# Performance work log

Hardware: AMD Instinct MI355X
Metric: run time of the kernel (lower is better)

Reference implementation:

```python
import jax, jax.numpy as jnp
import numpy as np

N = 100000   # nodes
E = 625000   # edges
H = 128      # hidden dim
G = 64       # graphs in batch
HOPS = 5
EPS = 1e-5


def _gelu(x):
    return jax.nn.gelu(x, approximate=False)  # torch nn.GELU default (exact erf)


def _bn(x, g, b):
    # BatchNorm1d in training mode: batch statistics, biased variance
    m = jnp.mean(x, axis=0)
    v = jnp.var(x, axis=0)
    return (x - m) * jax.lax.rsqrt(v + EPS) * g + b


def _ffnn(x, W1, b1, W2, b2):
    # Linear -> GELU -> Linear -> GELU
    return _gelu(_gelu(x @ W1 + b1) @ W2 + b2)


def _vn_mlp(x, W1, b1, g1, be1, W2, b2, g2, be2):
    # Linear -> BN -> GELU -> Linear -> BN -> GELU
    h = _gelu(_bn(x @ W1 + b1, g1, be1))
    return _gelu(_bn(h @ W2 + b2, g2, be2))


def _gcn(x, W, b, src, dst):
    # PyG GCNConv: xW, symmetric-normalized aggregation over edges w/ self loops, + bias
    h = x @ W
    deg = jax.ops.segment_sum(jnp.ones_like(src, dtype=h.dtype), dst, num_segments=N)
    dinv = jax.lax.rsqrt(jnp.maximum(deg, 1.0))  # deg >= 1 due to self loops
    norm = dinv[src] * dinv[dst]                 # [E+N]
    out = jax.ops.segment_sum(h[src] * norm[:, None], dst, num_segments=N)
    return out + b


def _forward(x, edge_index, batch, pre_W1, pre_b1, pre_W2, pre_b2, conv_W, conv_b,
             bn_g, bn_b, ffn_W1, ffn_b1, ffn_W2, ffn_b2, vn_W1, vn_b1, vn_g1, vn_be1,
             vn_W2, vn_b2, vn_g2, vn_be2, vn_emb, post_W1, post_b1, post_W2, post_b2):
    loop = jnp.arange(N)
    src = jnp.concatenate([edge_index[0], loop])
    dst = jnp.concatenate([edge_index[1], loop])

    x = _ffnn(x.astype(jnp.float32), pre_W1, pre_b1, pre_W2, pre_b2)
    vn = jnp.broadcast_to(vn_emb[0], (G, H))  # vn(zeros(num_graphs))

    counts = jax.ops.segment_sum(jnp.ones((N,), x.dtype), batch, num_segments=G)
    inv_counts = 1.0 / jnp.maximum(counts, 1.0)

    for i in range(HOPS):
        x = x + vn[batch]
        x = _gcn(x, conv_W[i], conv_b[i], src, dst) + x
        x = _bn(x, bn_g[i], bn_b[i])
        x = _ffnn(x, ffn_W1[i], ffn_b1[i], ffn_W2[i], ffn_b2[i]) + x
        # dropout p=0.0 -> identity
        if i < HOPS - 1:
            pooled = jax.ops.segment_sum(x, batch, num_segments=G) * inv_counts[:, None]
            vn = vn + pooled
            vn = _vn_mlp(vn, vn_W1[i], vn_b1[i], vn_g1[i], vn_be1[i],
                         vn_W2[i], vn_b2[i], vn_g2[i], vn_be2[i])

    x = jax.ops.segment_sum(x, batch, num_segments=G)  # global_add_pool
    return _ffnn(x, post_W1, post_b1, post_W2, post_b2)


def setup_inputs():
    key = jax.random.key(0)
    ks = iter(jax.random.split(key, 40))
    def nrm(shape, s=0.05):
        return jax.random.normal(next(ks), shape, dtype=jnp.float32) * s
    d = {}
    d["x"] = jax.random.normal(next(ks), (N, H), dtype=jnp.float32)
    d["edge_index"] = jax.random.randint(next(ks), (2, E), 0, N)
    d["batch"] = jnp.sort(jax.random.randint(next(ks), (N,), 0, G))
    d["pre_W1"] = nrm((H, 2 * H)); d["pre_b1"] = jnp.zeros((2 * H,), jnp.float32)
    d["pre_W2"] = nrm((2 * H, H)); d["pre_b2"] = jnp.zeros((H,), jnp.float32)
    d["conv_W"] = nrm((HOPS, H, H)); d["conv_b"] = jnp.zeros((HOPS, H), jnp.float32)
    d["bn_g"] = jnp.ones((HOPS, H), jnp.float32); d["bn_b"] = jnp.zeros((HOPS, H), jnp.float32)
    d["ffn_W1"] = nrm((HOPS, H, 2 * H)); d["ffn_b1"] = jnp.zeros((HOPS, 2 * H), jnp.float32)
    d["ffn_W2"] = nrm((HOPS, 2 * H, H)); d["ffn_b2"] = jnp.zeros((HOPS, H), jnp.float32)
    d["vn_W1"] = nrm((HOPS - 1, H, 2 * H)); d["vn_b1"] = jnp.zeros((HOPS - 1, 2 * H), jnp.float32)
    d["vn_g1"] = jnp.ones((HOPS - 1, 2 * H), jnp.float32); d["vn_be1"] = jnp.zeros((HOPS - 1, 2 * H), jnp.float32)
    d["vn_W2"] = nrm((HOPS - 1, 2 * H, H)); d["vn_b2"] = jnp.zeros((HOPS - 1, H), jnp.float32)
    d["vn_g2"] = jnp.ones((HOPS - 1, H), jnp.float32); d["vn_be2"] = jnp.zeros((HOPS - 1, H), jnp.float32)
    d["vn_emb"] = nrm((1, H))
    d["post_W1"] = nrm((H, 2 * H)); d["post_b1"] = jnp.zeros((2 * H,), jnp.float32)
    d["post_W2"] = nrm((2 * H, H)); d["post_b2"] = jnp.zeros((H,), jnp.float32)
    return d


def reference(x, edge_index, batch, pre_W1, pre_b1, pre_W2, pre_b2, conv_W, conv_b,
              bn_g, bn_b, ffn_W1, ffn_b1, ffn_W2, ffn_b2, vn_W1, vn_b1, vn_g1, vn_be1,
              vn_W2, vn_b2, vn_g2, vn_be2, vn_emb, post_W1, post_b1, post_W2, post_b2):
    return _forward(x, edge_index, batch, pre_W1, pre_b1, pre_W2, pre_b2, conv_W, conv_b,
                    bn_g, bn_b, ffn_W1, ffn_b1, ffn_W2, ffn_b2, vn_W1, vn_b1, vn_g1, vn_be1,
                    vn_W2, vn_b2, vn_g2, vn_be2, vn_emb, post_W1, post_b1, post_W2, post_b2)
```

## Files before the change

### kernel.cpp

```cpp
#include <hip/hip_runtime.h>
#include <math.h>

#define H 128
#define H2 256
#define LDC 136

typedef __attribute__((ext_vector_type(8))) short short8;
typedef __attribute__((ext_vector_type(4))) float floatx4;

__device__ __forceinline__ float gelu_f(float x) {
  float t = 1.59576912161f * x * fmaf(0.044715f, x * x, 1.0f);
  return x / (1.0f + __expf(-t));
}

__device__ __forceinline__ unsigned short f2b(float f) {
  union { float f; unsigned u; } c; c.f = f;
  unsigned r = c.u + 0x7fffu + ((c.u >> 16) & 1u);
  return (unsigned short)(r >> 16);
}

__device__ __forceinline__ float b2f(unsigned short u) {
  union { unsigned u; float f; } c; c.u = ((unsigned)u) << 16; return c.f;
}

__device__ __forceinline__ short8 pack8(floatx4 a, floatx4 b) {
  union { short8 v; unsigned short s[8]; } u;
  u.s[0] = f2b(a.x); u.s[1] = f2b(a.y); u.s[2] = f2b(a.z); u.s[3] = f2b(a.w);
  u.s[4] = f2b(b.x); u.s[5] = f2b(b.y); u.s[6] = f2b(b.z); u.s[7] = f2b(b.w);
  return u.v;
}

__global__ __launch_bounds__(256) void transpose_w(const float* __restrict__ W, unsigned short* __restrict__ WT,
                                                   int K, int Ncol, int total) {
  int i = blockIdx.x * 256 + threadIdx.x;
  if (i >= total) return;
  int kn = K * Ncol;
  int b = i / kn, r = i - b * kn;
  int k = r / Ncol, n = r - k * Ncol;
  WT[b * kn + n * K + k] = f2b(W[i]);
}


__global__ __launch_bounds__(256) void hist_kernel(int* __restrict__ cnt, const int* __restrict__ dst, int E) {
  int i = blockIdx.x * 256 + threadIdx.x;
  if (i < E) atomicAdd(&cnt[dst[i]], 1);
}

__global__ __launch_bounds__(256) void scan_a(const int* __restrict__ cnt, int* __restrict__ row_ptr,
                                              int* __restrict__ blockSum, float* __restrict__ dinv, int N) {
  __shared__ int ls[256];
  int t = threadIdx.x;
  int idx = blockIdx.x * 1024 + t * 4;
  int4 v = make_int4(0, 0, 0, 0);
  if (idx + 3 < N) v = *(const int4*)&cnt[idx];
  else {
    if (idx + 0 < N) v.x = cnt[idx + 0];
    if (idx + 1 < N) v.y = cnt[idx + 1];
    if (idx + 2 < N) v.z = cnt[idx + 2];
    if (idx + 3 < N) v.w = cnt[idx + 3];
  }
  if (idx + 0 < N) dinv[idx + 0] = rsqrtf((float)v.x + 1.0f);
  if (idx + 1 < N) dinv[idx + 1] = rsqrtf((float)v.y + 1.0f);
  if (idx + 2 < N) dinv[idx + 2] = rsqrtf((float)v.z + 1.0f);
  if (idx + 3 < N) dinv[idx + 3] = rsqrtf((float)v.w + 1.0f);
  int s = v.x + v.y + v.z + v.w;
  ls[t] = s;
  __syncthreads();
  for (int off = 1; off < 256; off <<= 1) {
    int a = (t >= off) ? ls[t - off] : 0;
    __syncthreads();
    ls[t] += a;
    __syncthreads();
  }
  int p = ls[t] - s;
  if (t == 255) blockSum[blockIdx.x] = ls[255];
  if (idx + 0 < N) row_ptr[idx + 0] = p;  p += v.x;
  if (idx + 1 < N) row_ptr[idx + 1] = p;  p += v.y;
  if (idx + 2 < N) row_ptr[idx + 2] = p;  p += v.z;
  if (idx + 3 < N) row_ptr[idx + 3] = p;
}

__global__ __launch_bounds__(1024) void scan_b(const int* __restrict__ blockSum, int* __restrict__ blockOff,
                                               int nb, int* __restrict__ row_ptr, int N, int E) {
  __shared__ int ls[1024];
  int t = threadIdx.x;
  int s = (t < nb) ? blockSum[t] : 0;
  ls[t] = s;
  __syncthreads();
  for (int off = 1; off < 1024; off <<= 1) {
    int a = (t >= off) ? ls[t - off] : 0;
    __syncthreads();
    ls[t] += a;
    __syncthreads();
  }
  if (t < nb) blockOff[t] = ls[t] - s;
  if (t == 0) row_ptr[N] = E;
}

__global__ __launch_bounds__(256) void scan_c(int* __restrict__ row_ptr, const int* __restrict__ blockOff, int N) {
  int t = threadIdx.x;
  int idx = blockIdx.x * 1024 + t * 4;
  int off = blockOff[blockIdx.x];
  if (off == 0) return;
  if (idx + 3 < N) {
    int4 v = *(const int4*)&row_ptr[idx];
    v.x += off; v.y += off; v.z += off; v.w += off;
    *(int4*)&row_ptr[idx] = v;
  } else {
    if (idx + 0 < N) row_ptr[idx + 0] += off;
    if (idx + 1 < N) row_ptr[idx + 1] += off;
    if (idx + 2 < N) row_ptr[idx + 2] += off;
    if (idx + 3 < N) row_ptr[idx + 3] += off;
  }
}

__global__ __launch_bounds__(256) void build_csr_kernel(const int* __restrict__ src, const int* __restrict__ dst,
                                                        const int* __restrict__ row_ptr, int* __restrict__ cursor,
                                                        const float* __restrict__ dinv,
                                                        int* __restrict__ csr_src, float* __restrict__ csr_norm,
                                                        int E) {
  int i = blockIdx.x * 256 + threadIdx.x;
  if (i < E) {
    int s = src[i], d = dst[i];
    int pos = row_ptr[d] + atomicAdd(&cursor[d], 1);
    csr_src[pos] = s;
    csr_norm[pos] = dinv[s] * dinv[d];
  }
}


__global__ __launch_bounds__(256) void count_kernel(float* counts, const int* __restrict__ batch, int N, int G) {
  __shared__ float hist[256];
  int t = threadIdx.x;
  if (t < G) hist[t] = 0.f;
  __syncthreads();
  int i0 = (blockIdx.x * 256 + t) * 16;
  int cur = -1; float run = 0.f;
  for (int j = 0; j < 16; j++) {
    int i = i0 + j;
    if (i < N) {
      int b = batch[i];
      if (b == cur) run += 1.f;
      else { if (cur >= 0) atomicAdd(&hist[cur], run); cur = b; run = 1.f; }
    }
  }
  if (cur >= 0) atomicAdd(&hist[cur], run);
  __syncthreads();
  if (t < G && hist[t] != 0.f) atomicAdd(&counts[t], hist[t]);
}

__global__ __launch_bounds__(256) void vn_init_kernel(float* vn, const float* __restrict__ emb, int n) {
  int i = blockIdx.x * 256 + threadIdx.x;
  if (i < n) vn[i] = emb[i & (H - 1)];
}

__global__ __launch_bounds__(256) void gather_agg(const unsigned short* __restrict__ h, const int* __restrict__ csr_src,
                                                  const float* __restrict__ csr_norm, const int* __restrict__ row_ptr,
                                                  const float* __restrict__ dinv, const float* __restrict__ vn,
                                                  const int* __restrict__ batch, const float* __restrict__ bias,
                                                  float* __restrict__ x, float* __restrict__ stats, int N) {
  __shared__ float sred[4 * H];
  __shared__ float qred[4 * H];
  int w = threadIdx.x >> 6, lane = threadIdx.x & 63;
  int c = lane * 2;
  float2 bi = *(const float2*)&bias[c];
  float s0t = 0.f, s1t = 0.f, q0t = 0.f, q1t = 0.f;
  int base = blockIdx.x * 32 + w * 8;
  for (int j = 0; j < 8; j++) {
    int node = base + j;
    if (node >= N) break;
    int b = batch[node];
    float di = dinv[node];
    float2 xo = *(const float2*)&x[(long)node * H + c];
    float2 vv = *(const float2*)&vn[b * H + c];
    unsigned hv = *(const unsigned*)&h[(long)node * H + c];
    int beg = row_ptr[node], end = row_ptr[node + 1];
    float ax = b2f((unsigned short)hv) * di * di;
    float ay = b2f((unsigned short)(hv >> 16)) * di * di;
    for (int e = beg; e < end; e += 8) {
      int si[8]; float wg[8]; unsigned u[8];
#pragma unroll
      for (int i = 0; i < 8; i++) {
        int ee = e + i;
        bool in = ee < end;
        int idx = in ? ee : beg;
        si[i] = csr_src[idx];
        wg[i] = in ? csr_norm[idx] : 0.f;
      }
#pragma unroll
      for (int i = 0; i < 8; i++) u[i] = *(const unsigned*)&h[(long)si[i] * H + c];
#pragma unroll
      for (int i = 0; i < 8; i++) {
        ax += b2f((unsigned short)u[i]) * wg[i];
        ay += b2f((unsigned short)(u[i] >> 16)) * wg[i];
      }
    }
    float rx = ax + xo.x + vv.x + bi.x;
    float ry = ay + xo.y + vv.y + bi.y;
    *(float2*)&x[(long)node * H + c] = make_float2(rx, ry);
    s0t += rx; q0t += rx * rx;
    s1t += ry; q1t += ry * ry;
  }
  sred[w * H + c] = s0t; sred[w * H + c + 1] = s1t;
  qred[w * H + c] = q0t; qred[w * H + c + 1] = q1t;
  __syncthreads();
  int t = threadIdx.x;
  if (t < H) {
    float s = sred[t] + sred[H + t] + sred[2 * H + t] + sred[3 * H + t];
    if (s != 0.f) atomicAdd(&stats[t], s);
  } else {
    int cc = t - H;
    float q = qred[cc] + qred[H + cc] + qred[2 * H + cc] + qred[3 * H + cc];
    if (q != 0.f) atomicAdd(&stats[H + cc], q);
  }
}

__global__ __launch_bounds__(128) void bn_finalize_kernel(const float* __restrict__ stats, const float* __restrict__ g,
                                                          const float* __restrict__ b, float* __restrict__ scsh,
                                                          float invN) {
  int c = threadIdx.x;
  float m = stats[c] * invN;
  float v = stats[H + c] * invN - m * m;
  float sc = rsqrtf(v + 1e-5f) * g[c];
  scsh[c] = sc;
  scsh[H + c] = b[c] - m * sc;
}

__global__ __launch_bounds__(256) void conv_gemm(const float* __restrict__ x, const unsigned short* __restrict__ BT,
                                                 const float* __restrict__ vn, const int* __restrict__ batch,
                                                 unsigned short* __restrict__ h16, int M) {
  __shared__ unsigned short Bs[H * LDC];
  int tid = threadIdx.x;
  int lane = tid & 63, w = tid >> 6;
  int row0 = blockIdx.x * 64;
  int mrow = lane & 15, quad = lane >> 4, cn = lane & 15;
  int arow = row0 + w * 16 + mrow;
  bool rin = arow < M;
  int b = rin ? batch[arow] : 0;

#pragma unroll
  for (int j = 0; j < 8; j++) {
    int chunk = j * 256 + tid;
    int n = chunk >> 4, k8 = (chunk & 15) * 8;
    *(short8*)&Bs[n * LDC + k8] = *(const short8*)&BT[(long)n * H + k8];
  }

  short8 af[4];
#pragma unroll
  for (int k0 = 0; k0 < 4; k0++) {
    int kb = k0 * 32 + quad * 8;
    floatx4 a0 = (floatx4)0.f, a1 = (floatx4)0.f;
    if (rin) {
      a0 = *(const floatx4*)&x[(long)arow * H + kb] + *(const floatx4*)&vn[b * H + kb];
      a1 = *(const floatx4*)&x[(long)arow * H + kb + 4] + *(const floatx4*)&vn[b * H + kb + 4];
    }
    af[k0] = pack8(a0, a1);
  }
  __syncthreads();

#pragma unroll
  for (int t = 0; t < 8; t++) {
    floatx4 a = (floatx4)0.f;
#pragma unroll
    for (int k0 = 0; k0 < 4; k0++) {
      int kb = k0 * 32 + quad * 8;
      short8 bf = *(const short8*)&Bs[(t * 16 + mrow) * LDC + kb];
      a = __builtin_amdgcn_mfma_f32_16x16x32_bf16(af[k0], bf, a, 0, 0, 0);
    }
    int c = t * 16 + cn;
#pragma unroll
    for (int i = 0; i < 4; i++) {
      int r = row0 + w * 16 + quad * 4 + i;
      if (r < M) h16[(long)r * H + c] = f2b(a[i]);
    }
  }
}

template <int BNRES, int POOL>
__global__ __launch_bounds__(1024) void ffn_persist(const float* __restrict__ A,
                                                    const unsigned short* __restrict__ W1T, const float* __restrict__ b1,
                                                    const unsigned short* __restrict__ W2T, const float* __restrict__ b2,
                                                    const float* __restrict__ scsh,
                                                    float* __restrict__ C, float* __restrict__ pooled,
                                                    const int* __restrict__ batch, int M) {
  __shared__ unsigned short lds[78848];
  int tid = threadIdx.x;
#pragma unroll
  for (int j = 0; j < 4; j++) {
    int idx = j * 1024 + tid;
    int n = idx >> 4, k8 = (idx & 15) * 8;
    *(short8*)&lds[n * 136 + k8] = *(const short8*)&W1T[n * 128 + k8];
  }
#pragma unroll
  for (int j = 0; j < 4; j++) {
    int idx = j * 1024 + tid;
    int n = idx >> 5, k8 = (idx & 31) * 8;
    *(short8*)&lds[34816 + n * 264 + k8] = *(const short8*)&W2T[n * 256 + k8];
  }
  __syncthreads();

  int lane = tid & 63, w = tid >> 6;
  int mrow = lane & 15, quad = lane >> 4, cn = lane & 15;
  unsigned short* scr = &lds[68608 + w * 640];
  int TT = (M + 15) >> 4;
  int stride = (int)(gridDim.x << 4);

  for (int tile = blockIdx.x * 16 + w; tile < TT; tile += stride) {
    int row0 = tile << 4;
    int arow = row0 + mrow;
    bool rin = arow < M;

    short8 af[4];
#pragma unroll
    for (int k0 = 0; k0 < 4; k0++) {
      int kb = k0 * 32 + quad * 8;
      floatx4 a0 = (floatx4)0.f, a1 = (floatx4)0.f;
      if (rin) {
        a0 = *(const floatx4*)&A[(long)arow * H + kb];
        a1 = *(const floatx4*)&A[(long)arow * H + kb + 4];
        if (BNRES) {
          a0 = a0 * *(const floatx4*)&scsh[kb] + *(const floatx4*)&scsh[H + kb];
          a1 = a1 * *(const floatx4*)&scsh[kb + 4] + *(const floatx4*)&scsh[H + kb + 4];
        }
      }
      af[k0] = pack8(a0, a1);
    }

    floatx4 acc2[8];
#pragma unroll
    for (int t = 0; t < 8; t++) acc2[t] = (floatx4)0.f;

#pragma unroll
    for (int p = 0; p < 8; p++) {
#pragma unroll
      for (int u = 0; u < 2; u++) {
        int t = p * 2 + u;
        floatx4 a = (floatx4)0.f;
#pragma unroll
        for (int k = 0; k < 4; k++) {
          short8 bf = *(const short8*)&lds[(t * 16 + mrow) * 136 + k * 32 + quad * 8];
          a = __builtin_amdgcn_mfma_f32_16x16x32_bf16(af[k], bf, a, 0, 0, 0);
        }
        float bb = b1[t * 16 + cn];
#pragma unroll
        for (int i = 0; i < 4; i++)
          scr[(quad * 4 + i) * 40 + u * 16 + cn] = f2b(gelu_f(a[i] + bb));
      }
      short8 hf = *(const short8*)&scr[mrow * 40 + quad * 8];
#pragma unroll
      for (int ct = 0; ct < 8; ct++) {
        short8 bf = *(const short8*)&lds[34816 + (ct * 16 + mrow) * 264 + p * 32 + quad * 8];
        acc2[ct] = __builtin_amdgcn_mfma_f32_16x16x32_bf16(hf, bf, acc2[ct], 0, 0, 0);
      }
    }

    int g0 = 0; bool same = true;
    if (POOL) {
      int rl = row0 + 15; if (rl >= M) rl = M - 1;
      g0 = batch[row0];
      same = (batch[rl] == g0);
    }
#pragma unroll
    for (int t = 0; t < 8; t++) {
      int c = t * 16 + cn;
      float bb = b2[c];
      float rsc = 0.f, rsh = 0.f;
      if (BNRES) { rsc = scsh[c]; rsh = scsh[H + c]; }
      float s = 0.f;
#pragma unroll
      for (int i = 0; i < 4; i++) {
        int r = row0 + quad * 4 + i;
        float v = 0.f;
        if (r < M) {
          long off = (long)r * H + c;
          v = gelu_f(acc2[t][i] + bb);
          if (BNRES) v += C[off] * rsc + rsh;
          C[off] = v;
          if (POOL && !same) atomicAdd(&pooled[batch[r] * H + c], v);
        }
        s += v;
      }
      if (POOL && same) {
        s += __shfl_xor(s, 16);
        s += __shfl_xor(s, 32);
        if (quad == 0) atomicAdd(&pooled[g0 * H + c], s);
      }
    }
  }
}

template <int BN, int UVN>
__global__ __launch_bounds__(256) void mlp64_l1(const float* __restrict__ vn, const float* __restrict__ pooled,
                                                const float* __restrict__ counts,
                                                const float* __restrict__ W1, const float* __restrict__ b1,
                                                const float* __restrict__ g1, const float* __restrict__ be1,
                                                float* __restrict__ h1) {
  __shared__ float u[64 * H];
  __shared__ float red[8 * 64];
  int t = threadIdx.x;
  for (int idx = t; idx < 64 * H; idx += 256) {
    float v = pooled[idx];
    if (UVN) v = vn[idx] + v / fmaxf(counts[idx >> 7], 1.0f);
    u[idx] = v;
  }
  __syncthreads();
  int tc = t & 63, tg = t >> 6;
  int c = blockIdx.x * 64 + tc;
  float acc[16];
  float bj = b1[c];
#pragma unroll
  for (int g = 0; g < 16; g++) acc[g] = bj;
  for (int k0 = 0; k0 < H; k0 += 4) {
    float w0 = W1[(k0 + 0) * H2 + c];
    float w1 = W1[(k0 + 1) * H2 + c];
    float w2 = W1[(k0 + 2) * H2 + c];
    float w3 = W1[(k0 + 3) * H2 + c];
#pragma unroll
    for (int g = 0; g < 16; g++) {
      float4 v = *(const float4*)&u[(tg * 16 + g) * H + k0];
      acc[g] += v.x * w0 + v.y * w1 + v.z * w2 + v.w * w3;
    }
  }
  float sc = 1.f, sh = 0.f;
  if (BN) {
    float s = 0.f, s2 = 0.f;
#pragma unroll
    for (int g = 0; g < 16; g++) { s += acc[g]; s2 += acc[g] * acc[g]; }
    red[tg * 64 + tc] = s;
    red[256 + tg * 64 + tc] = s2;
    __syncthreads();
    float st = red[tc] + red[64 + tc] + red[128 + tc] + red[192 + tc];
    float st2 = red[256 + tc] + red[320 + tc] + red[384 + tc] + red[448 + tc];
    float m = st * (1.f / 64.f);
    float var = st2 * (1.f / 64.f) - m * m;
    sc = rsqrtf(var + 1e-5f) * g1[c];
    sh = be1[c] - m * sc;
  }
#pragma unroll
  for (int g = 0; g < 16; g++) h1[(tg * 16 + g) * H2 + c] = gelu_f(acc[g] * sc + sh);
}

template <int BN>
__global__ __launch_bounds__(256) void mlp64_l2(const float* __restrict__ h1,
                                                const float* __restrict__ W2, const float* __restrict__ b2,
                                                const float* __restrict__ g2, const float* __restrict__ be2,
                                                float* __restrict__ outp) {
  __shared__ float red[8 * 64];
  int t = threadIdx.x;
  int tc = t & 63, tg = t >> 6;
  int c = blockIdx.x * 64 + tc;
  float acc[16];
  float bj = b2[c];
#pragma unroll
  for (int g = 0; g < 16; g++) acc[g] = bj;
  for (int k0 = 0; k0 < H2; k0 += 4) {
    float w0 = W2[(k0 + 0) * H + c];
    float w1 = W2[(k0 + 1) * H + c];
    float w2 = W2[(k0 + 2) * H + c];
    float w3 = W2[(k0 + 3) * H + c];
#pragma unroll
    for (int g = 0; g < 16; g++) {
      float4 v = *(const float4*)&h1[(tg * 16 + g) * H2 + k0];
      acc[g] += v.x * w0 + v.y * w1 + v.z * w2 + v.w * w3;
    }
  }
  float sc = 1.f, sh = 0.f;
  if (BN) {
    float s = 0.f, s2 = 0.f;
#pragma unroll
    for (int g = 0; g < 16; g++) { s += acc[g]; s2 += acc[g] * acc[g]; }
    red[tg * 64 + tc] = s;
    red[256 + tg * 64 + tc] = s2;
    __syncthreads();
    float st = red[tc] + red[64 + tc] + red[128 + tc] + red[192 + tc];
    float st2 = red[256 + tc] + red[320 + tc] + red[384 + tc] + red[448 + tc];
    float m = st * (1.f / 64.f);
    float var = st2 * (1.f / 64.f) - m * m;
    sc = rsqrtf(var + 1e-5f) * g2[c];
    sh = be2[c] - m * sc;
  }
#pragma unroll
  for (int g = 0; g < 16; g++) outp[(tg * 16 + g) * H + c] = gelu_f(acc[g] * sc + sh);
}


extern "C" void kernel_launch(void* const* d_in, const int* in_sizes, int n_in,
                              void* d_out, int out_size, void* d_ws, size_t ws_size,
                              hipStream_t stream) {
  const float* x_in   = (const float*)d_in[0];
  const int*   edge   = (const int*)d_in[1];
  const int*   batch  = (const int*)d_in[2];
  const float* pre_W1 = (const float*)d_in[3];
  const float* pre_b1 = (const float*)d_in[4];
  const float* pre_W2 = (const float*)d_in[5];
  const float* pre_b2 = (const float*)d_in[6];
  const float* conv_W = (const float*)d_in[7];
  const float* conv_b = (const float*)d_in[8];
  const float* bn_g   = (const float*)d_in[9];
  const float* bn_b   = (const float*)d_in[10];
  const float* ffn_W1 = (const float*)d_in[11];
  const float* ffn_b1 = (const float*)d_in[12];
  const float* ffn_W2 = (const float*)d_in[13];
  const float* ffn_b2 = (const float*)d_in[14];
  const float* vn_W1  = (const float*)d_in[15];
  const float* vn_b1  = (const float*)d_in[16];
  const float* vn_g1  = (const float*)d_in[17];
  const float* vn_be1 = (const float*)d_in[18];
  const float* vn_W2  = (const float*)d_in[19];
  const float* vn_b2  = (const float*)d_in[20];
  const float* vn_g2  = (const float*)d_in[21];
  const float* vn_be2 = (const float*)d_in[22];
  const float* vn_emb = (const float*)d_in[23];
  const float* post_W1= (const float*)d_in[24];
  const float* post_b1= (const float*)d_in[25];
  const float* post_W2= (const float*)d_in[26];
  const float* post_b2= (const float*)d_in[27];
  float* out = (float*)d_out;

  const int N    = in_sizes[2];
  const int E    = in_sizes[1] / 2;
  const int G    = out_size / H;
  const int HOPS = in_sizes[7] / (H * H);
  const int NH   = N * H;

  float* w = (float*)d_ws;
  float* buf_x  = w;  w += NH;
  float* buf_t  = w;  w += N * H2;
  unsigned short* buf_h16 = (unsigned short*)buf_t;
  float* dinv   = w;  w += N;
  float* counts = w;  w += G;
  float* stats  = w;  w += 2 * H;
  float* scsh   = w;  w += 2 * H;
  float* pooled = w;  w += G * H;
  float* vn     = w;  w += G * H;
  float* mlp_h1 = w;  w += G * H2;
  float* csr_norm = w; w += E;
  int* iw = (int*)w;
  int* cnt      = iw;  iw += N;
  int* row_ptr  = iw;  iw += N + 1;
  int* cursor   = iw;  iw += N;
  int* csr_src  = iw;  iw += E;
  int* blockSum = iw;  iw += 1024;
  int* blockOff = iw;  iw += 1024;
  unsigned short* wt = (unsigned short*)iw;
  unsigned short* preW1T = wt;  wt += H * H2;
  unsigned short* preW2T = wt;  wt += H2 * H;
  unsigned short* convT  = wt;  wt += HOPS * H * H;
  unsigned short* ffn1T  = wt;  wt += HOPS * H * H2;
  unsigned short* ffn2T  = wt;  wt += HOPS * H2 * H;

  const int* src = edge;
  const int* dst = edge + E;

  int gE  = (E + 255) / 256;
  int gM  = (N + 63) / 64;
  int nb  = (N + 1023) / 1024;
  float invN = 1.0f / (float)N;

  transpose_w<<<(H * H2 + 255) / 256, 256, 0, stream>>>(pre_W1, preW1T, H, H2, H * H2);
  transpose_w<<<(H2 * H + 255) / 256, 256, 0, stream>>>(pre_W2, preW2T, H2, H, H2 * H);
  transpose_w<<<(HOPS * H * H + 255) / 256, 256, 0, stream>>>(conv_W, convT, H, H, HOPS * H * H);
  transpose_w<<<(HOPS * H * H2 + 255) / 256, 256, 0, stream>>>(ffn_W1, ffn1T, H, H2, HOPS * H * H2);
  transpose_w<<<(HOPS * H2 * H + 255) / 256, 256, 0, stream>>>(ffn_W2, ffn2T, H2, H, HOPS * H2 * H);

  hipMemsetAsync(cnt, 0, N * sizeof(int), stream);
  hist_kernel<<<gE, 256, 0, stream>>>(cnt, dst, E);
  scan_a<<<nb, 256, 0, stream>>>(cnt, row_ptr, blockSum, dinv, N);
  scan_b<<<1, 1024, 0, stream>>>(blockSum, blockOff, nb, row_ptr, N, E);
  scan_c<<<nb, 256, 0, stream>>>(row_ptr, blockOff, N);
  hipMemsetAsync(cursor, 0, N * sizeof(int), stream);
  build_csr_kernel<<<gE, 256, 0, stream>>>(src, dst, row_ptr, cursor, dinv, csr_src, csr_norm, E);

  hipMemsetAsync(counts, 0, G * sizeof(float), stream);
  count_kernel<<<(N + 256 * 16 - 1) / (256 * 16), 256, 0, stream>>>(counts, batch, N, G);
  vn_init_kernel<<<(G * H + 255) / 256, 256, 0, stream>>>(vn, vn_emb, G * H);

  ffn_persist<0, 0><<<256, 1024, 0, stream>>>(x_in, preW1T, pre_b1, preW2T, pre_b2, nullptr,
                                              buf_x, nullptr, nullptr, N);

  for (int i = 0; i < HOPS; i++) {
    conv_gemm<<<gM, 256, 0, stream>>>(buf_x, convT + i * H * H, vn, batch, buf_h16, N);
    hipMemsetAsync(stats, 0, 2 * H * sizeof(float), stream);
    gather_agg<<<(N + 31) / 32, 256, 0, stream>>>(buf_h16, csr_src, csr_norm, row_ptr, dinv, vn, batch,
                                                  conv_b + i * H, buf_x, stats, N);
    bn_finalize_kernel<<<1, 128, 0, stream>>>(stats, bn_g + i * H, bn_b + i * H, scsh, invN);
    hipMemsetAsync(pooled, 0, G * H * sizeof(float), stream);
    ffn_persist<1, 1><<<256, 1024, 0, stream>>>(buf_x, ffn1T + i * H * H2, ffn_b1 + i * H2,
                                                ffn2T + i * H2 * H, ffn_b2 + i * H, scsh,
                                                buf_x, pooled, batch, N);
    if (i < HOPS - 1) {
      mlp64_l1<1, 1><<<H2 / 64, 256, 0, stream>>>(vn, pooled, counts,
                                                  vn_W1 + i * H * H2, vn_b1 + i * H2, vn_g1 + i * H2, vn_be1 + i * H2,
                                                  mlp_h1);
      mlp64_l2<1><<<H / 64, 256, 0, stream>>>(mlp_h1, vn_W2 + i * H2 * H, vn_b2 + i * H, vn_g2 + i * H, vn_be2 + i * H, vn);
    }
  }

  mlp64_l1<0, 0><<<H2 / 64, 256, 0, stream>>>(nullptr, pooled, nullptr, post_W1, post_b1, nullptr, nullptr, mlp_h1);
  mlp64_l2<0><<<H / 64, 256, 0, stream>>>(mlp_h1, post_W2, post_b2, nullptr, nullptr, out);
}
```

Baseline: 1.778 ms.

## Restructure gather aggregation for multi-node ILP and prefetch FFN tiles

The gather kernel now has each wave handle two nodes at once with 4-wide channel vectors. It processes four node groups per half-wave in an interleaved way, loading CSR indices cooperatively and broadcasting them with shuffles, so more independent gathers are in flight. conv_gemm issues its x loads before the weight staging into LDS. ffn_persist prefetches the next tile's A rows into registers and batches the residual reads and output stores, which overlaps global latency with MFMA work. The cost is higher register pressure, which may lower occupancy, plus some wasted loads on inactive lanes.

```diff
diff --git a/kernel.cpp b/kernel.cpp
--- a/kernel.cpp
+++ b/kernel.cpp
@@ -22,6 +22,9 @@
 __device__ __forceinline__ float b2f(unsigned short u) {
   union { unsigned u; float f; } c; c.u = ((unsigned)u) << 16; return c.f;
 }
+
+__device__ __forceinline__ float blo(unsigned u) { return __uint_as_float(u << 16); }
+__device__ __forceinline__ float bhi(unsigned u) { return __uint_as_float(u & 0xffff0000u); }
 
 __device__ __forceinline__ short8 pack8(floatx4 a, floatx4 b) {
   union { short8 v; unsigned short s[8]; } u;
@@ -162,47 +165,130 @@
   __shared__ float sred[4 * H];
   __shared__ float qred[4 * H];
   int w = threadIdx.x >> 6, lane = threadIdx.x & 63;
-  int c = lane * 2;
-  float2 bi = *(const float2*)&bias[c];
-  float s0t = 0.f, s1t = 0.f, q0t = 0.f, q1t = 0.f;
+  int hh = lane >> 5;
+  int li = lane & 31;
+  int c = li * 4;
+  floatx4 bi = *(const floatx4*)&bias[c];
   int base = blockIdx.x * 32 + w * 8;
-  for (int j = 0; j < 8; j++) {
-    int node = base + j;
-    if (node >= N) break;
-    int b = batch[node];
-    float di = dinv[node];
-    float2 xo = *(const float2*)&x[(long)node * H + c];
-    float2 vv = *(const float2*)&vn[b * H + c];
-    unsigned hv = *(const unsigned*)&h[(long)node * H + c];
-    int beg = row_ptr[node], end = row_ptr[node + 1];
-    float ax = b2f((unsigned short)hv) * di * di;
-    float ay = b2f((unsigned short)(hv >> 16)) * di * di;
-    for (int e = beg; e < end; e += 8) {
-      int si[8]; float wg[8]; unsigned u[8];
-#pragma unroll
-      for (int i = 0; i < 8; i++) {
-        int ee = e + i;
-        bool in = ee < end;
-        int idx = in ? ee : beg;
-        si[i] = csr_src[idx];
-        wg[i] = in ? csr_norm[idx] : 0.f;
+
+  int nd[4]; bool act[4];
+#pragma unroll
+  for (int j = 0; j < 4; j++) {
+    int n0 = base + 2 * j + hh;
+    act[j] = n0 < N;
+    nd[j] = act[j] ? n0 : (N - 1);
+  }
+  int beg[4], end[4], bt[4];
+  float dd[4];
+#pragma unroll
+  for (int j = 0; j < 4; j++) { beg[j] = row_ptr[nd[j]]; end[j] = row_ptr[nd[j] + 1]; }
+#pragma unroll
+  for (int j = 0; j < 4; j++) { bt[j] = batch[nd[j]]; float di = dinv[nd[j]]; dd[j] = di * di; }
+  floatx4 xo[4]; uint2 hs[4];
+#pragma unroll
+  for (int j = 0; j < 4; j++) {
+    xo[j] = *(const floatx4*)&x[(long)nd[j] * H + c];
+    hs[j] = *(const uint2*)&h[(long)nd[j] * H + c];
+  }
+  float a0[4], a1[4], a2[4], a3[4];
+#pragma unroll
+  for (int j = 0; j < 4; j++) {
+    a0[j] = blo(hs[j].x) * dd[j];
+    a1[j] = bhi(hs[j].x) * dd[j];
+    a2[j] = blo(hs[j].y) * dd[j];
+    a3[j] = bhi(hs[j].y) * dd[j];
+  }
+
+#define GROUP_CSR(j, eb, sv, nv)                      \
+  int sv; float nv;                                   \
+  {                                                   \
+    int idx_ = beg[j] + (eb) + li;                    \
+    bool vld_ = (li < 8) && (idx_ < end[j]);          \
+    int sidx_ = vld_ ? idx_ : 0;                      \
+    sv = csr_src[sidx_];                              \
+    nv = vld_ ? csr_norm[sidx_] : 0.f;                \
+  }
+
+#define GROUP_GACC(j, sv, nv)                         \
+  {                                                   \
+    uint2 u_[8]; float wg_[8];                        \
+    _Pragma("unroll")                                 \
+    for (int ii = 0; ii < 8; ii++) {                  \
+      wg_[ii] = __shfl(nv, hh * 32 + ii);             \
+      int si_ = __shfl(sv, hh * 32 + ii);             \
+      u_[ii] = *(const uint2*)&h[(long)si_ * H + c];  \
+    }                                                 \
+    _Pragma("unroll")                                 \
+    for (int ii = 0; ii < 8; ii++) {                  \
+      a0[j] += blo(u_[ii].x) * wg_[ii];               \
+      a1[j] += bhi(u_[ii].x) * wg_[ii];               \
+      a2[j] += blo(u_[ii].y) * wg_[ii];               \
+      a3[j] += bhi(u_[ii].y) * wg_[ii];               \
+    }                                                 \
+  }
+
+  {
+    GROUP_CSR(0, 0, sv0, nv0)
+    GROUP_CSR(1, 0, sv1, nv1)
+    GROUP_CSR(2, 0, sv2, nv2)
+    GROUP_CSR(3, 0, sv3, nv3)
+    GROUP_GACC(0, sv0, nv0)
+    GROUP_GACC(1, sv1, nv1)
+    GROUP_GACC(2, sv2, nv2)
+    GROUP_GACC(3, sv3, nv3)
+  }
+
+  int dmx[4];
+#pragma unroll
+  for (int j = 0; j < 4; j++) {
+    int d = end[j] - beg[j];
+    int dx = __shfl_xor(d, 32);
+    dmx[j] = d > dx ? d : dx;
+  }
+  int dall = dmx[0];
+  if (dmx[1] > dall) dall = dmx[1];
+  if (dmx[2] > dall) dall = dmx[2];
+  if (dmx[3] > dall) dall = dmx[3];
+  for (int eb = 8; eb < dall; eb += 8) {
+#pragma unroll
+    for (int j = 0; j < 4; j++) {
+      if (eb < dmx[j]) {
+        GROUP_CSR(j, eb, svt, nvt)
+        GROUP_GACC(j, svt, nvt)
       }
-#pragma unroll
-      for (int i = 0; i < 8; i++) u[i] = *(const unsigned*)&h[(long)si[i] * H + c];
-#pragma unroll
-      for (int i = 0; i < 8; i++) {
-        ax += b2f((unsigned short)u[i]) * wg[i];
-        ay += b2f((unsigned short)(u[i] >> 16)) * wg[i];
-      }
-    }
-    float rx = ax + xo.x + vv.x + bi.x;
-    float ry = ay + xo.y + vv.y + bi.y;
-    *(float2*)&x[(long)node * H + c] = make_float2(rx, ry);
-    s0t += rx; q0t += rx * rx;
-    s1t += ry; q1t += ry * ry;
-  }
-  sred[w * H + c] = s0t; sred[w * H + c + 1] = s1t;
-  qred[w * H + c] = q0t; qred[w * H + c + 1] = q1t;
+    }
+  }
+#undef GROUP_CSR
+#undef GROUP_GACC
+
+  float s0 = 0.f, s1 = 0.f, s2 = 0.f, s3 = 0.f;
+  float q0 = 0.f, q1 = 0.f, q2 = 0.f, q3 = 0.f;
+#pragma unroll
+  for (int j = 0; j < 4; j++) {
+    floatx4 vv = *(const floatx4*)&vn[bt[j] * H + c];
+    float r0 = a0[j] + xo[j].x + vv.x + bi.x;
+    float r1 = a1[j] + xo[j].y + vv.y + bi.y;
+    float r2 = a2[j] + xo[j].z + vv.z + bi.z;
+    float r3 = a3[j] + xo[j].w + vv.w + bi.w;
+    if (act[j]) {
+      floatx4 rv = {r0, r1, r2, r3};
+      *(floatx4*)&x[(long)nd[j] * H + c] = rv;
+      s0 += r0; q0 += r0 * r0;
+      s1 += r1; q1 += r1 * r1;
+      s2 += r2; q2 += r2 * r2;
+      s3 += r3; q3 += r3 * r3;
+    }
+  }
+  s0 += __shfl_xor(s0, 32); s1 += __shfl_xor(s1, 32);
+  s2 += __shfl_xor(s2, 32); s3 += __shfl_xor(s3, 32);
+  q0 += __shfl_xor(q0, 32); q1 += __shfl_xor(q1, 32);
+  q2 += __shfl_xor(q2, 32); q3 += __shfl_xor(q3, 32);
+  if (hh == 0) {
+    floatx4 sv4 = {s0, s1, s2, s3};
+    floatx4 qv4 = {q0, q1, q2, q3};
+    *(floatx4*)&sred[w * H + c] = sv4;
+    *(floatx4*)&qred[w * H + c] = qv4;
+  }
   __syncthreads();
   int t = threadIdx.x;
   if (t < H) {
@@ -238,6 +324,14 @@
   bool rin = arow < M;
   int b = rin ? batch[arow] : 0;
 
+  floatx4 xr[8];
+#pragma unroll
+  for (int k0 = 0; k0 < 4; k0++) {
+    int kb = k0 * 32 + quad * 8;
+    xr[2 * k0]     = rin ? *(const floatx4*)&x[(long)arow * H + kb]     : (floatx4)0.f;
+    xr[2 * k0 + 1] = rin ? *(const floatx4*)&x[(long)arow * H + kb + 4] : (floatx4)0.f;
+  }
+
 #pragma unroll
   for (int j = 0; j < 8; j++) {
     int chunk = j * 256 + tid;
@@ -249,15 +343,16 @@
 #pragma unroll
   for (int k0 = 0; k0 < 4; k0++) {
     int kb = k0 * 32 + quad * 8;
-    floatx4 a0 = (floatx4)0.f, a1 = (floatx4)0.f;
+    floatx4 a0 = xr[2 * k0], a1 = xr[2 * k0 + 1];
     if (rin) {
-      a0 = *(const floatx4*)&x[(long)arow * H + kb] + *(const floatx4*)&vn[b * H + kb];
-      a1 = *(const floatx4*)&x[(long)arow * H + kb + 4] + *(const floatx4*)&vn[b * H + kb + 4];
+      a0 = a0 + *(const floatx4*)&vn[b * H + kb];
+      a1 = a1 + *(const floatx4*)&vn[b * H + kb + 4];
     }
     af[k0] = pack8(a0, a1);
   }
   __syncthreads();
 
+  floatx4 aacc[8];
 #pragma unroll
   for (int t = 0; t < 8; t++) {
     floatx4 a = (floatx4)0.f;
@@ -267,11 +362,14 @@
       short8 bf = *(const short8*)&Bs[(t * 16 + mrow) * LDC + kb];
       a = __builtin_amdgcn_mfma_f32_16x16x32_bf16(af[k0], bf, a, 0, 0, 0);
     }
-    int c = t * 16 + cn;
-#pragma unroll
-    for (int i = 0; i < 4; i++) {
-      int r = row0 + w * 16 + quad * 4 + i;
-      if (r < M) h16[(long)r * H + c] = f2b(a[i]);
+    aacc[t] = a;
+  }
+#pragma unroll
+  for (int i = 0; i < 4; i++) {
+    int r = row0 + w * 16 + quad * 4 + i;
+    if (r < M) {
+#pragma unroll
+      for (int t = 0; t < 8; t++) h16[(long)r * H + t * 16 + cn] = f2b(aacc[t][i]);
     }
   }
 }
@@ -285,6 +383,24 @@
                                                     const int* __restrict__ batch, int M) {
   __shared__ unsigned short lds[78848];
   int tid = threadIdx.x;
+  int lane = tid & 63, w = tid >> 6;
+  int mrow = lane & 15, quad = lane >> 4, cn = lane & 15;
+  int TT = (M + 15) >> 4;
+  int stride = (int)(gridDim.x << 4);
+  int tile = blockIdx.x * 16 + w;
+
+  floatx4 ar[8];
+  {
+    int arow = (tile << 4) + mrow;
+    bool v = (tile < TT) && (arow < M);
+#pragma unroll
+    for (int k0 = 0; k0 < 4; k0++) {
+      int kb = k0 * 32 + quad * 8;
+      ar[2 * k0]     = v ? *(const floatx4*)&A[(long)arow * H + kb]     : (floatx4)0.f;
+      ar[2 * k0 + 1] = v ? *(const floatx4*)&A[(long)arow * H + kb + 4] : (floatx4)0.f;
+    }
+  }
+
 #pragma unroll
   for (int j = 0; j < 4; j++) {
     int idx = j * 1024 + tid;
@@ -299,31 +415,34 @@
   }
   __syncthreads();
 
-  int lane = tid & 63, w = tid >> 6;
-  int mrow = lane & 15, quad = lane >> 4, cn = lane & 15;
   unsigned short* scr = &lds[68608 + w * 640];
-  int TT = (M + 15) >> 4;
-  int stride = (int)(gridDim.x << 4);
-
-  for (int tile = blockIdx.x * 16 + w; tile < TT; tile += stride) {
+
+  for (; tile < TT; tile += stride) {
     int row0 = tile << 4;
-    int arow = row0 + mrow;
-    bool rin = arow < M;
 
     short8 af[4];
 #pragma unroll
     for (int k0 = 0; k0 < 4; k0++) {
       int kb = k0 * 32 + quad * 8;
-      floatx4 a0 = (floatx4)0.f, a1 = (floatx4)0.f;
-      if (rin) {
-        a0 = *(const floatx4*)&A[(long)arow * H + kb];
-        a1 = *(const floatx4*)&A[(long)arow * H + kb + 4];
-        if (BNRES) {
-          a0 = a0 * *(const floatx4*)&scsh[kb] + *(const floatx4*)&scsh[H + kb];
-          a1 = a1 * *(const floatx4*)&scsh[kb + 4] + *(const floatx4*)&scsh[H + kb + 4];
-        }
+      floatx4 a0 = ar[2 * k0], a1 = ar[2 * k0 + 1];
+      if (BNRES) {
+        a0 = a0 * *(const floatx4*)&scsh[kb] + *(const floatx4*)&scsh[H + kb];
+        a1 = a1 * *(const floatx4*)&scsh[kb + 4] + *(const floatx4*)&scsh[H + kb + 4];
       }
       af[k0] = pack8(a0, a1);
+    }
+
+    floatx4 nx[8];
+    {
+      int nt = tile + stride;
+      int arow = (nt << 4) + mrow;
+      bool v = (nt < TT) && (arow < M);
+#pragma unroll
+      for (int k0 = 0; k0 < 4; k0++) {
+        int kb = k0 * 32 + quad * 8;
+        nx[2 * k0]     = v ? *(const floatx4*)&A[(long)arow * H + kb]     : (floatx4)0.f;
+        nx[2 * k0 + 1] = v ? *(const floatx4*)&A[(long)arow * H + kb + 4] : (floatx4)0.f;
+      }
     }
 
     floatx4 acc2[8];
@@ -354,38 +473,60 @@
       }
     }
 
-    int g0 = 0; bool same = true;
+    float res[4][8];
+    if (BNRES) {
+#pragma unroll
+      for (int i = 0; i < 4; i++) {
+        int r = row0 + quad * 4 + i;
+        bool rv = r < M;
+#pragma unroll
+        for (int t = 0; t < 8; t++)
+          res[i][t] = rv ? C[(long)r * H + t * 16 + cn] : 0.f;
+      }
+    }
+
+    int g0v = 0; bool same = true;
     if (POOL) {
       int rl = row0 + 15; if (rl >= M) rl = M - 1;
-      g0 = batch[row0];
-      same = (batch[rl] == g0);
-    }
+      g0v = batch[row0];
+      same = (batch[rl] == g0v);
+    }
+    float bbv[8], rscv[8], rshv[8], sp[8];
 #pragma unroll
     for (int t = 0; t < 8; t++) {
-      int c = t * 16 + cn;
-      float bb = b2[c];
-      float rsc = 0.f, rsh = 0.f;
-      if (BNRES) { rsc = scsh[c]; rsh = scsh[H + c]; }
-      float s = 0.f;
-#pragma unroll
-      for (int i = 0; i < 4; i++) {
-        int r = row0 + quad * 4 + i;
-        float v = 0.f;
-        if (r < M) {
-          long off = (long)r * H + c;
-          v = gelu_f(acc2[t][i] + bb);
-          if (BNRES) v += C[off] * rsc + rsh;
-          C[off] = v;
-          if (POOL && !same) atomicAdd(&pooled[batch[r] * H + c], v);
+      int cc = t * 16 + cn;
+      bbv[t] = b2[cc];
+      rscv[t] = BNRES ? scsh[cc] : 0.f;
+      rshv[t] = BNRES ? scsh[H + cc] : 0.f;
+      sp[t] = 0.f;
+    }
+#pragma unroll
+    for (int i = 0; i < 4; i++) {
+      int r = row0 + quad * 4 + i;
+      bool rv = r < M;
+#pragma unroll
+      for (int t = 0; t < 8; t++) {
+        float v = gelu_f(acc2[t][i] + bbv[t]);
+        if (BNRES) v += res[i][t] * rscv[t] + rshv[t];
+        v = rv ? v : 0.f;
+        if (rv) {
+          C[(long)r * H + t * 16 + cn] = v;
+          if (POOL && !same) atomicAdd(&pooled[batch[r] * H + t * 16 + cn], v);
         }
-        s += v;
+        sp[t] += v;
       }
-      if (POOL && same) {
+    }
+    if (POOL && same) {
+#pragma unroll
+      for (int t = 0; t < 8; t++) {
+        float s = sp[t];
         s += __shfl_xor(s, 16);
         s += __shfl_xor(s, 32);
-        if (quad == 0) atomicAdd(&pooled[g0 * H + c], s);
+        if (quad == 0) atomicAdd(&pooled[g0v * H + t * 16 + cn], s);
       }
     }
+#pragma unroll
+    for (int q = 0; q < 8; q++) ar[q] = nx[q];
   }
 }
 
```

After: 2.094 ms. +17.8%, slower.
